# Performance work log

Measured on AMD Instinct MI355X. Metric: run time of the kernel, lower is better.

Reference implementation:

```python
import jax, jax.numpy as jnp
import numpy as np

NEG_INF = -1.0e15  # matches the module's self.infty


def setup_inputs() -> dict:
    key = jax.random.key(0)
    ks = jax.random.split(key, 12)
    B, N, D, H, HD = 256, 1024, 128, 8, 16
    inp = {
        "x": jax.random.normal(ks[0], (B, N, D), dtype=jnp.float32),
        "h_g": jax.random.normal(ks[1], (B, D), dtype=jnp.float32),
        "first": jax.random.normal(ks[2], (B, D), dtype=jnp.float32),
        "last": jax.random.normal(ks[3], (B, D), dtype=jnp.float32),
        "context": jax.random.normal(ks[4], (B, 2), dtype=jnp.float32),
        "K": jax.random.normal(ks[5], (B, H, N, HD), dtype=jnp.float32),
        "V": jax.random.normal(ks[6], (B, H, N, HD), dtype=jnp.float32),
        "K_lg": jax.random.normal(ks[7], (B, N, D), dtype=jnp.float32),
        "Wq": jax.random.normal(ks[8], (D, 3 * D + 2), dtype=jnp.float32) * 0.05,
        "bq": jnp.zeros((D,), dtype=jnp.float32),
        "Wo": jax.random.normal(ks[9], (D, D), dtype=jnp.float32) * 0.05,
        "bo": jnp.zeros((D,), dtype=jnp.float32),
        "mask": jax.random.randint(ks[10], (B, N), 0, 2, dtype=jnp.int32),
        "t": 1,
    }
    return inp


def reference(x, h_g, first, last, context, K, V, K_lg, Wq, bq, Wo, bo, mask, t):
    B, N, D = x.shape
    H, HD = K.shape[1], K.shape[3]
    # t > 0 path: context vector from graph embedding + first/last visited nodes
    h_c = jnp.concatenate([h_g, first, last, context], axis=1)  # [B, 3D+2]
    Q = h_c @ Wq.T + bq                                          # [B, D]
    Q = Q.reshape(B, H, HD)                                      # single query per head
    # masked single-query multi-head attention
    scale = jnp.sqrt(jnp.asarray(HD, dtype=x.dtype))
    scores = jnp.einsum("bhd,bhnd->bhn", Q, K) / scale          # [B, H, N]
    scores = jnp.where(mask[:, None, :] == 0, NEG_INF, scores)
    attn = jax.nn.softmax(scores, axis=-1)
    u = jnp.einsum("bhn,bhnd->bhd", attn, V).reshape(B, D)       # [B, D]
    u = u @ Wo.T + bo
    # pointer logits with tanh clipping
    logits = jnp.einsum("bd,bnd->bn", u, K_lg) / jnp.sqrt(jnp.asarray(D, dtype=x.dtype))
    logits = 10.0 * jnp.tanh(logits)
    logits = jnp.where(mask == 0, NEG_INF, logits)
    p = jax.nn.softmax(logits, axis=1)                           # [B, N]
    vertexes = jnp.argmax(p, axis=1)[:, None]                    # greedy (sample=False)
    probs = jnp.take_along_axis(p, vertexes, axis=1)             # [B, 1]
    return vertexes, probs
```

## Files before the change

kernel.cpp:

```cpp
#include <hip/hip_runtime.h>
#include <math.h>

#define Bn 256
#define Nn 1024
#define Dn 128
#define Hn 8
#define HDn 16
#define NEG_INF -1.0e15f

typedef float v4f __attribute__((ext_vector_type(4)));

__global__ __launch_bounds__(128) void k_q(
    const float* __restrict__ h_g, const float* __restrict__ first,
    const float* __restrict__ last, const float* __restrict__ context,
    const float* __restrict__ Wq, const float* __restrict__ bq,
    float* __restrict__ Qout)
{
    __shared__ __align__(16) float hc[3 * Dn + 2];
    const int b = blockIdx.x;
    const int t = threadIdx.x;
    hc[t]          = h_g[b * Dn + t];
    hc[Dn + t]     = first[b * Dn + t];
    hc[2 * Dn + t] = last[b * Dn + t];
    if (t < 2) hc[3 * Dn + t] = context[b * 2 + t];
    __syncthreads();

    const float2* w2 = (const float2*)(Wq + (size_t)t * (3 * Dn + 2));
    const float2* h2 = (const float2*)hc;
    float acc = bq[t];
#pragma unroll 8
    for (int k = 0; k < (3 * Dn + 2) / 2; ++k) {
        float2 w = w2[k], h = h2[k];
        acc = fmaf(w.x, h.x, fmaf(w.y, h.y, acc));
    }
    Qout[b * Dn + t] = acc;
}

__global__ __launch_bounds__(1024) void k_attn(
    const float* __restrict__ Q, const float* __restrict__ K,
    const float* __restrict__ V, const int* __restrict__ mask,
    float* __restrict__ Uout)
{
    __shared__ __align__(16) float sPart[16][Hn][20];
    __shared__ __align__(16) float sTot[Hn][20];

    const int b = blockIdx.x;
    const int tid = threadIdx.x;
    const int lane = tid & 63, wave = tid >> 6;
    const int g = tid & 3;
    const int kq = tid >> 2;

    const int* __restrict__ mrow = mask + (size_t)b * Nn;
    int mk[4];
#pragma unroll
    for (int p = 0; p < 4; ++p) mk[p] = mrow[p * 256 + kq];

    const float4* __restrict__ Qrow = (const float4*)(Q + (size_t)b * Dn);
    const float4* __restrict__ Kb = (const float4*)(K + (size_t)b * Hn * Nn * HDn);
    const v4f*    __restrict__ Vb = (const v4f*)(V + (size_t)b * Hn * Nn * HDn);

#pragma unroll
    for (int s = 0; s < Hn; ++s) {
        const float4 qg = Qrow[s * 4 + g];
        const float4* __restrict__ Kh = Kb + (size_t)s * 4096;
        const v4f*    __restrict__ Vh = Vb + (size_t)s * 4096;

        float4 kf[4];
        v4f vf[4];
#pragma unroll
        for (int p = 0; p < 4; ++p) kf[p] = Kh[p * 1024 + tid];
#pragma unroll
        for (int p = 0; p < 4; ++p) vf[p] = __builtin_nontemporal_load(&Vh[p * 1024 + tid]);
        __builtin_amdgcn_sched_barrier(0);

        float4 u = {0.f, 0.f, 0.f, 0.f};
        float sum = 0.f;
#pragma unroll
        for (int p = 0; p < 4; ++p) {
            float sc = qg.x * kf[p].x + qg.y * kf[p].y + qg.z * kf[p].z + qg.w * kf[p].w;
            sc += __shfl_xor(sc, 1, 64);
            sc += __shfl_xor(sc, 2, 64);
            const float e = mk[p] ? __expf(sc * 0.25f) : 0.f;
            sum += e;
            u.x = fmaf(e, vf[p].x, u.x);
            u.y = fmaf(e, vf[p].y, u.y);
            u.z = fmaf(e, vf[p].z, u.z);
            u.w = fmaf(e, vf[p].w, u.w);
        }
#pragma unroll
        for (int o = 4; o <= 32; o <<= 1) {
            u.x += __shfl_xor(u.x, o, 64);
            u.y += __shfl_xor(u.y, o, 64);
            u.z += __shfl_xor(u.z, o, 64);
            u.w += __shfl_xor(u.w, o, 64);
            sum += __shfl_xor(sum, o, 64);
        }
        if (lane < 4) *(float4*)(&sPart[wave][s][lane * 4]) = u;
        if (lane == 0) sPart[wave][s][16] = sum;
    }
    __syncthreads();

    if (tid < Hn * 17) {
        const int s = tid / 17, j = tid % 17;
        float a = 0.f;
#pragma unroll
        for (int w = 0; w < 16; ++w) a += sPart[w][s][j];
        sTot[s][j] = a;
    }
    __syncthreads();
    if (tid < Dn) {
        const int s = tid >> 4, j = tid & 15;
        Uout[(size_t)b * Dn + tid] = sTot[s][j] / sTot[s][16];
    }
}

__global__ __launch_bounds__(1024) void k_ptr(
    const float* __restrict__ U, const float* __restrict__ Wo,
    const float* __restrict__ bo, const float* __restrict__ K_lg,
    const int* __restrict__ mask, float* __restrict__ out)
{
    __shared__ __align__(16) float sU[Dn];
    __shared__ __align__(16) float sU2[Dn];
    __shared__ __align__(16) float sL[Nn];
    __shared__ float sRv[16];
    __shared__ int   sRi[16];
    __shared__ float sRs[16];

    const int b = blockIdx.x;
    const int tid = threadIdx.x;
    const int lane = tid & 63, wave = tid >> 6;

    if (tid < Dn) sU[tid] = U[b * Dn + tid];
    __syncthreads();
    {
        const int d = tid >> 3, e8 = tid & 7;
        const float4* wrow = (const float4*)(Wo + (size_t)d * Dn + e8 * 16);
        const float4* su4 = (const float4*)(sU + e8 * 16);
        float acc = 0.f;
#pragma unroll
        for (int k = 0; k < 4; ++k) {
            const float4 w = wrow[k], u = su4[k];
            acc = fmaf(w.x, u.x, fmaf(w.y, u.y, fmaf(w.z, u.z, fmaf(w.w, u.w, acc))));
        }
        acc += __shfl_xor(acc, 1, 64);
        acc += __shfl_xor(acc, 2, 64);
        acc += __shfl_xor(acc, 4, 64);
        if (e8 == 0) sU2[d] = acc + bo[d];
    }
    __syncthreads();

    const float4* __restrict__ Kl = (const float4*)(K_lg + (size_t)b * Nn * Dn);
    const int* __restrict__ mrow = mask + (size_t)b * Nn;
    const int grp = tid >> 5, l32 = tid & 31;
    const float4 u2f = ((const float4*)sU2)[l32];
    const float sc = 0.08838834764831845f;
#pragma unroll
    for (int it0 = 0; it0 < 32; it0 += 4) {
        float4 kl[4];
#pragma unroll
        for (int j = 0; j < 4; ++j)
            kl[j] = Kl[(size_t)(grp + 32 * (it0 + j)) * 32 + l32];
        __builtin_amdgcn_sched_barrier(0);
#pragma unroll
        for (int j = 0; j < 4; ++j) {
            float p = kl[j].x * u2f.x + kl[j].y * u2f.y + kl[j].z * u2f.z + kl[j].w * u2f.w;
#pragma unroll
            for (int o = 16; o >= 1; o >>= 1) p += __shfl_xor(p, o, 64);
            if (l32 == 0) {
                const int n = grp + 32 * (it0 + j);
                sL[n] = (mrow[n] == 0) ? NEG_INF : 10.0f * tanhf(p * sc);
            }
        }
    }
    __syncthreads();

    float bv = sL[tid]; int bi = tid;
#pragma unroll
    for (int o = 32; o >= 1; o >>= 1) {
        const float ov = __shfl_xor(bv, o, 64);
        const int oi = __shfl_xor(bi, o, 64);
        if (ov > bv || (ov == bv && oi < bi)) { bv = ov; bi = oi; }
    }
    if (lane == 0) { sRv[wave] = bv; sRi[wave] = bi; }
    __syncthreads();
    bv = sRv[0]; bi = sRi[0];
#pragma unroll
    for (int w = 1; w < 16; ++w) {
        const float ov = sRv[w]; const int oi = sRi[w];
        if (ov > bv || (ov == bv && oi < bi)) { bv = ov; bi = oi; }
    }

    float lsum = __expf(sL[tid] - bv);
#pragma unroll
    for (int o = 32; o >= 1; o >>= 1) lsum += __shfl_xor(lsum, o, 64);
    if (lane == 0) sRs[wave] = lsum;
    __syncthreads();
    if (tid == 0) {
        float tot = 0.f;
#pragma unroll
        for (int w = 0; w < 16; ++w) tot += sRs[w];
        out[b] = (float)bi;
        out[Bn + b] = 1.0f / tot;
    }
}

extern "C" void kernel_launch(void* const* d_in, const int* in_sizes, int n_in,
                              void* d_out, int out_size, void* d_ws, size_t ws_size,
                              hipStream_t stream) {
    const float* h_g     = (const float*)d_in[1];
    const float* first   = (const float*)d_in[2];
    const float* last    = (const float*)d_in[3];
    const float* context = (const float*)d_in[4];
    const float* K       = (const float*)d_in[5];
    const float* V       = (const float*)d_in[6];
    const float* K_lg    = (const float*)d_in[7];
    const float* Wq      = (const float*)d_in[8];
    const float* bq      = (const float*)d_in[9];
    const float* Wo      = (const float*)d_in[10];
    const float* bo      = (const float*)d_in[11];
    const int*   mask    = (const int*)d_in[12];
    float* out = (float*)d_out;

    float* Qws = (float*)d_ws;
    float* Uws = Qws + Bn * Dn;

    k_q   <<<Bn,  128, 0, stream>>>(h_g, first, last, context, Wq, bq, Qws);
    k_attn<<<Bn, 1024, 0, stream>>>(Qws, K, V, mask, Uws);
    k_ptr <<<Bn, 1024, 0, stream>>>(Uws, Wo, bo, K_lg, mask, out);
}
```

Measured before the change: 101.6 us.

## Split attention kernel into separate score and weighted-V kernels

Splits the fused attention kernel into two kernels. The first computes the masked exponentiated scores and writes them to a workspace buffer. The second reads those scores back and accumulates them against V. This lowers register pressure and shortens the load chains in each kernel, at the cost of an extra launch and an 8 MB workspace round trip through memory.

```diff
diff --git a/kernel.cpp b/kernel.cpp
--- a/kernel.cpp
+++ b/kernel.cpp
@@ -36,19 +36,13 @@
     Qout[b * Dn + t] = acc;
 }
 
-__global__ __launch_bounds__(1024) void k_attn(
+__global__ __launch_bounds__(1024) void k_score(
     const float* __restrict__ Q, const float* __restrict__ K,
-    const float* __restrict__ V, const int* __restrict__ mask,
-    float* __restrict__ Uout)
-{
-    __shared__ __align__(16) float sPart[16][Hn][20];
-    __shared__ __align__(16) float sTot[Hn][20];
-
+    const int* __restrict__ mask, float* __restrict__ Ews)
+{
     const int b = blockIdx.x;
     const int tid = threadIdx.x;
-    const int lane = tid & 63, wave = tid >> 6;
-    const int g = tid & 3;
-    const int kq = tid >> 2;
+    const int g = tid & 3, kq = tid >> 2;
 
     const int* __restrict__ mrow = mask + (size_t)b * Nn;
     int mk[4];
@@ -57,35 +51,66 @@
 
     const float4* __restrict__ Qrow = (const float4*)(Q + (size_t)b * Dn);
     const float4* __restrict__ Kb = (const float4*)(K + (size_t)b * Hn * Nn * HDn);
-    const v4f*    __restrict__ Vb = (const v4f*)(V + (size_t)b * Hn * Nn * HDn);
+    float* __restrict__ ebase = Ews + (size_t)b * Hn * Nn;
 
 #pragma unroll
     for (int s = 0; s < Hn; ++s) {
         const float4 qg = Qrow[s * 4 + g];
         const float4* __restrict__ Kh = Kb + (size_t)s * 4096;
-        const v4f*    __restrict__ Vh = Vb + (size_t)s * 4096;
-
         float4 kf[4];
-        v4f vf[4];
 #pragma unroll
         for (int p = 0; p < 4; ++p) kf[p] = Kh[p * 1024 + tid];
-#pragma unroll
-        for (int p = 0; p < 4; ++p) vf[p] = __builtin_nontemporal_load(&Vh[p * 1024 + tid]);
         __builtin_amdgcn_sched_barrier(0);
-
-        float4 u = {0.f, 0.f, 0.f, 0.f};
-        float sum = 0.f;
+        float e[4];
 #pragma unroll
         for (int p = 0; p < 4; ++p) {
             float sc = qg.x * kf[p].x + qg.y * kf[p].y + qg.z * kf[p].z + qg.w * kf[p].w;
             sc += __shfl_xor(sc, 1, 64);
             sc += __shfl_xor(sc, 2, 64);
-            const float e = mk[p] ? __expf(sc * 0.25f) : 0.f;
-            sum += e;
-            u.x = fmaf(e, vf[p].x, u.x);
-            u.y = fmaf(e, vf[p].y, u.y);
-            u.z = fmaf(e, vf[p].z, u.z);
-            u.w = fmaf(e, vf[p].w, u.w);
+            e[p] = mk[p] ? __expf(sc * 0.25f) : 0.f;
+        }
+        if (g == 0) {
+#pragma unroll
+            for (int p = 0; p < 4; ++p) ebase[s * Nn + p * 256 + kq] = e[p];
+        }
+    }
+}
+
+__global__ __launch_bounds__(1024) void k_av(
+    const float* __restrict__ Ews, const float* __restrict__ V,
+    float* __restrict__ Uout)
+{
+    __shared__ __align__(16) float sPart[16][Hn][20];
+    __shared__ __align__(16) float sTot[Hn][20];
+
+    const int b = blockIdx.x;
+    const int tid = threadIdx.x;
+    const int lane = tid & 63, wave = tid >> 6;
+    const int g = tid & 3, kq = tid >> 2;
+
+    const v4f* __restrict__ Vb = (const v4f*)(V + (size_t)b * Hn * Nn * HDn);
+    const float* __restrict__ ebase = Ews + (size_t)b * Hn * Nn;
+
+#pragma unroll
+    for (int s = 0; s < Hn; ++s) {
+        const v4f* __restrict__ Vh = Vb + (size_t)s * 4096;
+        v4f vf[4];
+        float e[4];
+#pragma unroll
+        for (int p = 0; p < 4; ++p) vf[p] = __builtin_nontemporal_load(&Vh[p * 1024 + tid]);
+#pragma unroll
+        for (int p = 0; p < 4; ++p) e[p] = ebase[s * Nn + p * 256 + kq];
+        __builtin_amdgcn_sched_barrier(0);
+
+        float4 u = {0.f, 0.f, 0.f, 0.f};
+        float sum = 0.f;
+#pragma unroll
+        for (int p = 0; p < 4; ++p) {
+            sum += e[p];
+            u.x = fmaf(e[p], vf[p].x, u.x);
+            u.y = fmaf(e[p], vf[p].y, u.y);
+            u.z = fmaf(e[p], vf[p].z, u.z);
+            u.w = fmaf(e[p], vf[p].w, u.w);
         }
 #pragma unroll
         for (int o = 4; o <= 32; o <<= 1) {
@@ -223,8 +248,10 @@
 
     float* Qws = (float*)d_ws;
     float* Uws = Qws + Bn * Dn;
-
-    k_q   <<<Bn,  128, 0, stream>>>(h_g, first, last, context, Wq, bq, Qws);
-    k_attn<<<Bn, 1024, 0, stream>>>(Qws, K, V, mask, Uws);
-    k_ptr <<<Bn, 1024, 0, stream>>>(Uws, Wo, bo, K_lg, mask, out);
-}
+    float* Ews = Uws + Bn * Dn;
+
+    k_q    <<<Bn,  128, 0, stream>>>(h_g, first, last, context, Wq, bq, Qws);
+    k_score<<<Bn, 1024, 0, stream>>>(Qws, K, mask, Ews);
+    k_av   <<<Bn, 1024, 0, stream>>>(Ews, V, Uws);
+    k_ptr  <<<Bn, 1024, 0, stream>>>(Uws, Wo, bo, K_lg, mask, out);
+}
```

Measured after the change: 106.2 us. 1.05x slower.

## Split attention into score and AV kernels with atomic accumulation across grid

Applied to the files above, without the earlier changes.

Replaces the per-batch attention kernel (256 blocks of 1024 threads) with two grid-strided kernels of 2048 blocks each. The first computes masked exp-scores into a workspace, and the second multiplies them by V and accumulates per-head partial sums with global atomics. Accumulator zeroing moves into the Q kernel, and the pointer kernel does the normalization. This aims for more parallelism and better load balance across CUs, at the cost of an extra kernel launch, an extra workspace round trip for the scores, and heavy atomic traffic.

```diff
diff --git a/kernel.cpp b/kernel.cpp
--- a/kernel.cpp
+++ b/kernel.cpp
@@ -10,15 +10,21 @@
 
 typedef float v4f __attribute__((ext_vector_type(4)));
 
+#define ACC_FLOATS (Bn * Hn * 20)
+
 __global__ __launch_bounds__(128) void k_q(
     const float* __restrict__ h_g, const float* __restrict__ first,
     const float* __restrict__ last, const float* __restrict__ context,
     const float* __restrict__ Wq, const float* __restrict__ bq,
-    float* __restrict__ Qout)
+    float* __restrict__ Qout, float* __restrict__ Acc)
 {
     __shared__ __align__(16) float hc[3 * Dn + 2];
     const int b = blockIdx.x;
     const int t = threadIdx.x;
+
+    const int z = (b * 128 + t) * 2;
+    if (z < ACC_FLOATS) { Acc[z] = 0.f; Acc[z + 1] = 0.f; }
+
     hc[t]          = h_g[b * Dn + t];
     hc[Dn + t]     = first[b * Dn + t];
     hc[2 * Dn + t] = last[b * Dn + t];
@@ -36,86 +42,74 @@
     Qout[b * Dn + t] = acc;
 }
 
-__global__ __launch_bounds__(1024) void k_attn(
+__global__ __launch_bounds__(256) void k_score(
     const float* __restrict__ Q, const float* __restrict__ K,
-    const float* __restrict__ V, const int* __restrict__ mask,
-    float* __restrict__ Uout)
-{
-    __shared__ __align__(16) float sPart[16][Hn][20];
-    __shared__ __align__(16) float sTot[Hn][20];
-
-    const int b = blockIdx.x;
+    const int* __restrict__ mask, float* __restrict__ Ews)
+{
     const int tid = threadIdx.x;
-    const int lane = tid & 63, wave = tid >> 6;
-    const int g = tid & 3;
-    const int kq = tid >> 2;
-
-    const int* __restrict__ mrow = mask + (size_t)b * Nn;
-    int mk[4];
-#pragma unroll
-    for (int p = 0; p < 4; ++p) mk[p] = mrow[p * 256 + kq];
-
-    const float4* __restrict__ Qrow = (const float4*)(Q + (size_t)b * Dn);
-    const float4* __restrict__ Kb = (const float4*)(K + (size_t)b * Hn * Nn * HDn);
-    const v4f*    __restrict__ Vb = (const v4f*)(V + (size_t)b * Hn * Nn * HDn);
-
-#pragma unroll
-    for (int s = 0; s < Hn; ++s) {
-        const float4 qg = Qrow[s * 4 + g];
-        const float4* __restrict__ Kh = Kb + (size_t)s * 4096;
-        const v4f*    __restrict__ Vh = Vb + (size_t)s * 4096;
-
-        float4 kf[4];
-        v4f vf[4];
-#pragma unroll
-        for (int p = 0; p < 4; ++p) kf[p] = Kh[p * 1024 + tid];
-#pragma unroll
-        for (int p = 0; p < 4; ++p) vf[p] = __builtin_nontemporal_load(&Vh[p * 1024 + tid]);
-        __builtin_amdgcn_sched_barrier(0);
-
-        float4 u = {0.f, 0.f, 0.f, 0.f};
-        float sum = 0.f;
-#pragma unroll
-        for (int p = 0; p < 4; ++p) {
-            float sc = qg.x * kf[p].x + qg.y * kf[p].y + qg.z * kf[p].z + qg.w * kf[p].w;
-            sc += __shfl_xor(sc, 1, 64);
-            sc += __shfl_xor(sc, 2, 64);
-            const float e = mk[p] ? __expf(sc * 0.25f) : 0.f;
-            sum += e;
-            u.x = fmaf(e, vf[p].x, u.x);
-            u.y = fmaf(e, vf[p].y, u.y);
-            u.z = fmaf(e, vf[p].z, u.z);
-            u.w = fmaf(e, vf[p].w, u.w);
-        }
+    const int lane = tid & 63;
+    const int g = lane & 3;
+    const long long idx0 = (long long)blockIdx.x * 256 + tid;
+    const float4* __restrict__ K4 = (const float4*)K;
+    const float4* __restrict__ Q4 = (const float4*)Q;
+
+#pragma unroll
+    for (int step = 0; step < 16; ++step) {
+        const long long idx = idx0 + (long long)step * 524288;
+        const long long key = idx >> 2;
+        const int bh = (int)(idx >> 12);
+        const int n = (int)(key & (Nn - 1));
+        const int b = bh >> 3;
+        const float4 kf = K4[idx];
+        const float4 qf = Q4[bh * 4 + g];
+        float sc = qf.x * kf.x + qf.y * kf.y + qf.z * kf.z + qf.w * kf.w;
+        sc += __shfl_xor(sc, 1, 64);
+        sc += __shfl_xor(sc, 2, 64);
+        const float e = mask[b * Nn + n] ? __expf(sc * 0.25f) : 0.f;
+        if (g == 0) Ews[key] = e;
+    }
+}
+
+__global__ __launch_bounds__(256) void k_av(
+    const float* __restrict__ Ews, const float* __restrict__ V,
+    float* __restrict__ Acc)
+{
+    const int tid = threadIdx.x;
+    const int lane = tid & 63;
+    const int g = lane & 3;
+    const long long idx0 = (long long)blockIdx.x * 256 + tid;
+    const v4f* __restrict__ V4 = (const v4f*)V;
+
+#pragma unroll
+    for (int step = 0; step < 16; ++step) {
+        const long long idx = idx0 + (long long)step * 524288;
+        const long long key = idx >> 2;
+        const int bh = (int)(idx >> 12);
+        const v4f vf = __builtin_nontemporal_load(&V4[idx]);
+        const float e = Ews[key];
+        float cx = e * vf.x, cy = e * vf.y, cz = e * vf.z, cw = e * vf.w;
+        float es = (g == 0) ? e : 0.f;
 #pragma unroll
         for (int o = 4; o <= 32; o <<= 1) {
-            u.x += __shfl_xor(u.x, o, 64);
-            u.y += __shfl_xor(u.y, o, 64);
-            u.z += __shfl_xor(u.z, o, 64);
-            u.w += __shfl_xor(u.w, o, 64);
-            sum += __shfl_xor(sum, o, 64);
-        }
-        if (lane < 4) *(float4*)(&sPart[wave][s][lane * 4]) = u;
-        if (lane == 0) sPart[wave][s][16] = sum;
-    }
-    __syncthreads();
-
-    if (tid < Hn * 17) {
-        const int s = tid / 17, j = tid % 17;
-        float a = 0.f;
-#pragma unroll
-        for (int w = 0; w < 16; ++w) a += sPart[w][s][j];
-        sTot[s][j] = a;
-    }
-    __syncthreads();
-    if (tid < Dn) {
-        const int s = tid >> 4, j = tid & 15;
-        Uout[(size_t)b * Dn + tid] = sTot[s][j] / sTot[s][16];
+            cx += __shfl_xor(cx, o, 64);
+            cy += __shfl_xor(cy, o, 64);
+            cz += __shfl_xor(cz, o, 64);
+            cw += __shfl_xor(cw, o, 64);
+            es += __shfl_xor(es, o, 64);
+        }
+        if (lane < 4) {
+            float* a = Acc + (size_t)bh * 20 + lane * 4;
+            atomicAdd(a + 0, cx);
+            atomicAdd(a + 1, cy);
+            atomicAdd(a + 2, cz);
+            atomicAdd(a + 3, cw);
+        }
+        if (lane == 0) atomicAdd(Acc + (size_t)bh * 20 + 16, es);
     }
 }
 
 __global__ __launch_bounds__(1024) void k_ptr(
-    const float* __restrict__ U, const float* __restrict__ Wo,
+    const float* __restrict__ Acc, const float* __restrict__ Wo,
     const float* __restrict__ bo, const float* __restrict__ K_lg,
     const int* __restrict__ mask, float* __restrict__ out)
 {
@@ -130,7 +124,10 @@
     const int tid = threadIdx.x;
     const int lane = tid & 63, wave = tid >> 6;
 
-    if (tid < Dn) sU[tid] = U[b * Dn + tid];
+    if (tid < Dn) {
+        const float* a = Acc + ((size_t)b * Hn + (tid >> 4)) * 20;
+        sU[tid] = a[tid & 15] / a[16];
+    }
     __syncthreads();
     {
         const int d = tid >> 3, e8 = tid & 7;
@@ -222,9 +219,11 @@
     float* out = (float*)d_out;
 
     float* Qws = (float*)d_ws;
-    float* Uws = Qws + Bn * Dn;
-
-    k_q   <<<Bn,  128, 0, stream>>>(h_g, first, last, context, Wq, bq, Qws);
-    k_attn<<<Bn, 1024, 0, stream>>>(Qws, K, V, mask, Uws);
-    k_ptr <<<Bn, 1024, 0, stream>>>(Uws, Wo, bo, K_lg, mask, out);
-}
+    float* Ews = Qws + Bn * Dn;
+    float* Acc = Ews + Bn * Hn * Nn;
+
+    k_q    <<<Bn,   128, 0, stream>>>(h_g, first, last, context, Wq, bq, Qws, Acc);
+    k_score<<<2048, 256, 0, stream>>>(Qws, K, mask, Ews);
+    k_av   <<<2048, 256, 0, stream>>>(Ews, V, Acc);
+    k_ptr  <<<Bn,  1024, 0, stream>>>(Acc, Wo, bo, K_lg, mask, out);
+}
```

Measured after the change: 181.7 us. 78.9% more time.
